# Optimization experiments

Hardware: AMD Instinct MI355X
Metric: run time of the kernel (lower is better)

## Reference

```python
import jax, jax.numpy as jnp
import numpy as np

B_SZ = 64            # oft_block_size
IN_F = 4096
OUT_F = 4096
R_IN = IN_F // B_SZ   # 64 blocks
R_OUT = OUT_F // B_SZ # 64 blocks
N_TRI = B_SZ * (B_SZ - 1) // 2  # 2016 packed strict-upper entries
NUM_NEUMANN = 5

_rows, _cols = np.triu_indices(B_SZ, k=1)
ROWS = jnp.asarray(_rows, dtype=jnp.int32)
COLS = jnp.asarray(_cols, dtype=jnp.int32)


def setup_inputs() -> dict:
    key = jax.random.key(0)
    k = jax.random.split(key, 5)
    x = jax.random.normal(k[0], (4, 2048, IN_F), dtype=jnp.float32)
    # small skew entries so the Neumann series approximates the Cayley transform
    Ro = jax.random.normal(k[1], (R_OUT, N_TRI), dtype=jnp.float32) * 0.01
    Ri = jax.random.normal(k[2], (R_IN, N_TRI), dtype=jnp.float32) * 0.01
    W = jax.random.normal(k[3], (OUT_F, IN_F), dtype=jnp.float32) * (1.0 / np.sqrt(IN_F))
    bias = jax.random.normal(k[4], (OUT_F,), dtype=jnp.float32) * 0.01
    rng = np.random.default_rng(0)
    perm_in = rng.permutation(IN_F)
    perm_in_inv = np.argsort(perm_in)
    perm_out = rng.permutation(OUT_F)
    return {
        "x": x, "Ro": Ro, "Ri": Ri, "W": W, "bias": bias,
        "perm_in_inv": jnp.asarray(perm_in_inv, dtype=jnp.int32),
        "perm_out": jnp.asarray(perm_out, dtype=jnp.int32),
    }


def _skew(vec):
    # vec: (r, n_tri) packed strict-upper entries -> (r, b, b) skew-symmetric
    r = vec.shape[0]
    M = jnp.zeros((r, B_SZ, B_SZ), dtype=vec.dtype).at[:, ROWS, COLS].set(vec)
    return M - jnp.swapaxes(M, -2, -1)


def _cayley_neumann(Q):
    # R = I + 2*(Q + Q^2 + Q^3 + Q^4)   (num_neumann_terms = 5)
    I = jnp.eye(B_SZ, dtype=Q.dtype)
    acc = Q
    Qp = Q
    for _ in range(3, NUM_NEUMANN):
        pass
    Q2 = jnp.matmul(Q, Q)
    acc = acc + Q2
    Qp = Q2
    for _ in range(3, NUM_NEUMANN):
        Qp = jnp.matmul(Qp, Q)
        acc = acc + Qp
    return I + 2.0 * acc


def reference(x, Ro, Ri, W, bias, perm_in_inv, perm_out):
    R_out = _cayley_neumann(_skew(Ro))   # (r_out, b, b)
    R_in = _cayley_neumann(_skew(Ri))    # (r_in, b, b)

    B, S, _ = x.shape
    xp = x[..., perm_in_inv]                               # input permutation
    xb = xp.reshape(B, S, R_IN, B_SZ)
    xR = jnp.einsum('bsrc,rcd->bsrd', xb, R_in)            # block-diag right rotate
    y = xR.reshape(B, S, IN_F) @ W.T + bias                # base linear
    yb = y.reshape(B, S, R_OUT, B_SZ)
    yR = jnp.einsum('bsrc,rcd->bsrd', yb, R_out)           # block-diag output rotate
    out = yR.reshape(B, S, OUT_F)[..., perm_out]           # output permutation
    return out
```

## Files before the change

kernel.cpp:

```cpp
#include <hip/hip_runtime.h>
#include <stdint.h>

#define IN_F 4096
#define OUT_F 4096
#define NTRI 2016

typedef unsigned short u16;
typedef __attribute__((ext_vector_type(8))) short short8;
typedef __attribute__((ext_vector_type(4))) float f32x4;
typedef __attribute__((ext_vector_type(4))) unsigned short u16x4;

__device__ __forceinline__ u16 f2bf(float f) {
    uint32_t u = __builtin_bit_cast(uint32_t, f);
    u = (u + 0x7FFFu + ((u >> 16) & 1u)) >> 16;
    return (u16)u;
}

__device__ __forceinline__ void gload16(const void* g, void* l) {
    __builtin_amdgcn_global_load_lds((__attribute__((address_space(1))) void*)g,
                                     (__attribute__((address_space(3))) void*)l,
                                     16, 0, 0);
}

#define FENCE() asm volatile("" ::: "memory")

__global__ void k_inv_perm(const int* __restrict__ perm_in_inv,
                           const int* __restrict__ perm_out,
                           int* __restrict__ pin, int* __restrict__ pinv_out) {
    int i = blockIdx.x * 256 + threadIdx.x;
    if (i < IN_F) {
        pin[perm_in_inv[i]] = i;
        pinv_out[perm_out[i]] = i;
    }
}

__global__ __launch_bounds__(256) void k_cayley(const float* __restrict__ Ro,
                                                const float* __restrict__ Ri,
                                                float* __restrict__ Rout,
                                                u16* __restrict__ QT16,
                                                u16* __restrict__ P16) {
    __shared__ __align__(16) float Qs[64 * 64];
    __shared__ __align__(16) float Ps[64 * 68];
    __shared__ __align__(16) float Ts[64 * 68];
    int b = blockIdx.x;
    const float* vec = (b < 64) ? (Ro + (size_t)b * NTRI) : (Ri + (size_t)(b - 64) * NTRI);
    int t = threadIdx.x;
    int tr = t >> 4, tc = t & 15;
#pragma unroll
    for (int e = 0; e < 16; ++e) {
        int el = e * 256 + t;
        int i = el >> 6, j = el & 63;
        float q = 0.f;
        if (i < j) q =  vec[i * 63 - (i * (i - 1)) / 2 + (j - i - 1)];
        if (i > j) q = -vec[j * 63 - (j * (j - 1)) / 2 + (i - j - 1)];
        Qs[el] = q;
    }
    __syncthreads();
    float a2[4][4], a3[4][4], a4[4][4];
#pragma unroll
    for (int i = 0; i < 4; ++i)
#pragma unroll
        for (int j = 0; j < 4; ++j) { a2[i][j] = 0.f; a3[i][j] = 0.f; a4[i][j] = 0.f; }
    for (int k = 0; k < 64; ++k) {
        f32x4 qa = *(const f32x4*)&Qs[k * 64 + tr * 4];
        f32x4 qb = *(const f32x4*)&Qs[k * 64 + tc * 4];
#pragma unroll
        for (int i = 0; i < 4; ++i)
#pragma unroll
            for (int j = 0; j < 4; ++j) a2[i][j] -= qa[i] * qb[j];
    }
#pragma unroll
    for (int i = 0; i < 4; ++i)
#pragma unroll
        for (int j = 0; j < 4; ++j) Ps[(tr * 4 + i) * 68 + tc * 4 + j] = a2[i][j];
    __syncthreads();
    for (int k = 0; k < 64; ++k) {
        f32x4 pa = *(const f32x4*)&Ps[k * 68 + tr * 4];
        f32x4 qb = *(const f32x4*)&Qs[k * 64 + tc * 4];
#pragma unroll
        for (int i = 0; i < 4; ++i)
#pragma unroll
            for (int j = 0; j < 4; ++j) a3[i][j] += pa[i] * qb[j];
    }
#pragma unroll
    for (int i = 0; i < 4; ++i)
#pragma unroll
        for (int j = 0; j < 4; ++j) Ts[(tc * 4 + j) * 68 + tr * 4 + i] = -a3[i][j];
    __syncthreads();
    for (int k = 0; k < 64; ++k) {
        f32x4 ta = *(const f32x4*)&Ts[k * 68 + tr * 4];
        f32x4 qb = *(const f32x4*)&Qs[k * 64 + tc * 4];
#pragma unroll
        for (int i = 0; i < 4; ++i)
#pragma unroll
            for (int j = 0; j < 4; ++j) a4[i][j] -= ta[i] * qb[j];
    }
    if (b < 64) {
        float* dst = Rout + (size_t)b * 4096;
        u16* qt = QT16 + (size_t)b * 4096;
#pragma unroll
        for (int i = 0; i < 4; ++i) {
            int gi = tr * 4 + i;
            f32x4 q4 = *(const f32x4*)&Qs[gi * 64 + tc * 4];
            f32x4 o;
#pragma unroll
            for (int j = 0; j < 4; ++j) {
                int gj = tc * 4 + j;
                o[j] = 2.f * (q4[j] + a2[i][j] + a3[i][j] + a4[i][j]) + ((gi == gj) ? 1.f : 0.f);
            }
            *(f32x4*)&dst[gi * 64 + tc * 4] = o;
#pragma unroll
            for (int j = 0; j < 4; ++j) qt[(tc * 4 + j) * 64 + gi] = f2bf(o[j]);
        }
    } else {
        u16* p = P16 + (size_t)(b - 64) * 4096;
#pragma unroll
        for (int i = 0; i < 4; ++i) {
            int gi = tr * 4 + i;
            f32x4 q4 = *(const f32x4*)&Qs[gi * 64 + tc * 4];
            u16x4 pk;
#pragma unroll
            for (int j = 0; j < 4; ++j) {
                int gj = tc * 4 + j;
                float v = 2.f * (q4[j] + a2[i][j] + a3[i][j] + a4[i][j]) + ((gi == gj) ? 1.f : 0.f);
                pk[j] = f2bf(v);
            }
            *(u16x4*)&p[gi * 64 + tc * 4] = pk;
        }
    }
}

__global__ void k_bias_rot(const float* __restrict__ bias, const float* __restrict__ Rout,
                           float* __restrict__ bias_prime) {
    int r = blockIdx.x;
    int d = threadIdx.x;
    const float* Rb = Rout + (size_t)r * 4096;
    float s = 0.f;
    for (int c = 0; c < 64; ++c) s += bias[r * 64 + c] * Rb[c * 64 + d];
    bias_prime[r * 64 + d] = s;
}

__global__ __launch_bounds__(256) void k_fold(const float* __restrict__ W,
                                              const u16* __restrict__ P16,
                                              const u16* __restrict__ QT16,
                                              const int* __restrict__ pinv_out,
                                              u16* __restrict__ Ctp) {
    __shared__ __align__(16) u16 Wst[128 * 64];
    __shared__ __align__(16) u16 Ut[64 * 128];
    const int s = blockIdx.x;
    const int br = blockIdx.y;
    const int t = threadIdx.x;
    const int lane = t & 63;
    const int w = t >> 6;
    const int fl = lane & 15;
    const int kg = lane >> 4;

    short8 bfP[4][2];
    const u16* Pbase = P16 + (size_t)s * 4096;
#pragma unroll
    for (int nf = 0; nf < 4; ++nf)
#pragma unroll
        for (int kk = 0; kk < 2; ++kk)
            bfP[nf][kk] = *(const short8*)(Pbase + (nf * 16 + fl) * 64 + kk * 32 + kg * 8);

#pragma unroll
    for (int q = 0; q < 4; ++q) {
        int ci = q * 256 + t;
        int row = ci >> 3, slot = ci & 7;
        const float* src = W + (size_t)(br * 128 + row) * IN_F + s * 64 + slot * 8;
        f32x4 v0 = *(const f32x4*)src;
        f32x4 v1 = *(const f32x4*)(src + 4);
        union { short8 v; u16 e[8]; } cv;
        cv.e[0] = f2bf(v0[0]); cv.e[1] = f2bf(v0[1]); cv.e[2] = f2bf(v0[2]); cv.e[3] = f2bf(v0[3]);
        cv.e[4] = f2bf(v1[0]); cv.e[5] = f2bf(v1[1]); cv.e[6] = f2bf(v1[2]); cv.e[7] = f2bf(v1[3]);
        *(short8*)&Wst[row * 64 + (slot ^ (row & 7)) * 8] = cv.v;
    }
    __syncthreads();

    f32x4 acc1[2][4];
#pragma unroll
    for (int mf = 0; mf < 2; ++mf)
#pragma unroll
        for (int nf = 0; nf < 4; ++nf) acc1[mf][nf] = f32x4{0.f, 0.f, 0.f, 0.f};
#pragma unroll
    for (int mf = 0; mf < 2; ++mf) {
        int row = w * 32 + mf * 16 + fl;
#pragma unroll
        for (int kk = 0; kk < 2; ++kk) {
            short8 a = *(const short8*)&Wst[row * 64 + ((kk * 4 + kg) ^ (row & 7)) * 8];
#pragma unroll
            for (int nf = 0; nf < 4; ++nf)
                acc1[mf][nf] = __builtin_amdgcn_mfma_f32_16x16x32_bf16(a, bfP[nf][kk], acc1[mf][nf], 0, 0, 0);
        }
    }
#pragma unroll
    for (int mf = 0; mf < 2; ++mf)
#pragma unroll
        for (int nf = 0; nf < 4; ++nf) {
            int i = nf * 16 + fl;
            int c = w * 32 + mf * 16 + kg * 4;
            u16x4 pk;
#pragma unroll
            for (int reg = 0; reg < 4; ++reg) pk[reg] = f2bf(acc1[mf][nf][reg]);
            int slot = c >> 3, half = (c >> 2) & 1;
            *(u16x4*)&Ut[i * 128 + ((slot ^ (i & 7)) << 3) + (half << 2)] = pk;
        }
    __syncthreads();

    const int rbl = w >> 1;
    const int r_g = br * 2 + rbl;
    short8 aQ[2][2];
#pragma unroll
    for (int mf2 = 0; mf2 < 2; ++mf2) {
        int d = (w & 1) * 32 + mf2 * 16 + fl;
#pragma unroll
        for (int kk = 0; kk < 2; ++kk)
            aQ[mf2][kk] = *(const short8*)(QT16 + (size_t)r_g * 4096 + d * 64 + kk * 32 + kg * 8);
    }
    f32x4 acc2[2][4];
#pragma unroll
    for (int mf2 = 0; mf2 < 2; ++mf2)
#pragma unroll
        for (int nf = 0; nf < 4; ++nf) acc2[mf2][nf] = f32x4{0.f, 0.f, 0.f, 0.f};
#pragma unroll
    for (int kk = 0; kk < 2; ++kk)
#pragma unroll
        for (int nf = 0; nf < 4; ++nf) {
            int i = nf * 16 + fl;
            int slot = rbl * 8 + kk * 4 + kg;
            short8 bu = *(const short8*)&Ut[i * 128 + ((slot ^ (i & 7)) << 3)];
#pragma unroll
            for (int mf2 = 0; mf2 < 2; ++mf2)
                acc2[mf2][nf] = __builtin_amdgcn_mfma_f32_16x16x32_bf16(aQ[mf2][kk], bu, acc2[mf2][nf], 0, 0, 0);
        }
#pragma unroll
    for (int mf2 = 0; mf2 < 2; ++mf2)
#pragma unroll
        for (int reg = 0; reg < 4; ++reg) {
            int o_g = br * 128 + w * 32 + mf2 * 16 + kg * 4 + reg;
            int j = pinv_out[o_g];
            u16* dst = Ctp + (size_t)j * IN_F + s * 64;
#pragma unroll
            for (int nf = 0; nf < 4; ++nf)
                dst[nf * 16 + fl] = f2bf(acc2[mf2][nf][reg]);
        }
}

__global__ __launch_bounds__(256) void k_permM(const u16* __restrict__ Ctp,
                                               const int* __restrict__ pin,
                                               u16* __restrict__ Mt) {
    __shared__ u16 row[4096];
    int j = blockIdx.x;
    int t = threadIdx.x;
    const u16* sr = Ctp + (size_t)j * IN_F;
#pragma unroll
    for (int e = 0; e < 16; ++e) row[e * 256 + t] = sr[e * 256 + t];
    __syncthreads();
    u16* dr = Mt + (size_t)j * IN_F;
#pragma unroll
    for (int e = 0; e < 16; ++e) {
        int k = e * 256 + t;
        dr[k] = row[pin[k]];
    }
}

__global__ void k_bias_perm(const float* __restrict__ bias_prime, const int* __restrict__ pout,
                            float* __restrict__ bias_final) {
    int j = blockIdx.x * 256 + threadIdx.x;
    if (j < OUT_F) bias_final[j] = bias_prime[pout[j]];
}

__global__ __launch_bounds__(256) void k_xcast(const float* __restrict__ x,
                                               u16* __restrict__ xb) {
    size_t idx = ((size_t)blockIdx.x * 256 + threadIdx.x) * 8;
    const f32x4* xp = (const f32x4*)(x + idx);
    f32x4 a = xp[0], b = xp[1];
    union { short8 v; u16 s[8]; } o;
    o.s[0] = f2bf(a[0]); o.s[1] = f2bf(a[1]); o.s[2] = f2bf(a[2]); o.s[3] = f2bf(a[3]);
    o.s[4] = f2bf(b[0]); o.s[5] = f2bf(b[1]); o.s[6] = f2bf(b[2]); o.s[7] = f2bf(b[3]);
    *(short8*)(xb + idx) = o.v;
}

__global__ __launch_bounds__(512, 2) void k_gemm(const u16* __restrict__ A,
                                                 const u16* __restrict__ Bt,
                                                 const float* __restrict__ bias,
                                                 float* __restrict__ out) {
    __shared__ __align__(16) u16 lds[65536];
    const int t = threadIdx.x;
    const int lane = t & 63;
    const int wid = t >> 6;
    const int wr = wid >> 2, wc = wid & 3;

    int flat = blockIdx.y * gridDim.x + blockIdx.x;
    int swz  = (flat & 7) * 64 + (flat >> 3);
    int bm = swz >> 4;
    int bn = swz & 15;

    const int srow = t >> 2;
    const int sks  = (t & 3) ^ ((t >> 3) & 3);
    const u16* sA0 = A  + (size_t)(bm * 256 + srow) * IN_F + sks * 8;
    const u16* sA1 = sA0 + (size_t)128 * IN_F;
    const u16* sB0 = Bt + (size_t)(bn * 256 + srow) * IN_F + sks * 8;
    const u16* sB1 = sB0 + (size_t)128 * IN_F;
    u16* dA = lds + t * 8;
    u16* dB = lds + 8192 + t * 8;

    const int frow = lane & 15;
    const int kg = lane >> 4;
    const int swzr = kg ^ ((frow >> 1) & 3);
    const int aoff = (wr * 128 + frow) * 32 + swzr * 8;
    const int boff = 8192 + (wc * 64 + frow) * 32 + swzr * 8;

    f32x4 acc[8][4];
#pragma unroll
    for (int m = 0; m < 8; ++m)
#pragma unroll
        for (int n = 0; n < 4; ++n) acc[m][n] = f32x4{0.f, 0.f, 0.f, 0.f};

#pragma unroll
    for (int p = 0; p < 3; ++p) {
        int off = p * 32;
        int bb = p * 16384;
        gload16(sA0 + off, dA + bb); gload16(sA1 + off, dA + bb + 4096);
        gload16(sB0 + off, dB + bb); gload16(sB1 + off, dB + bb + 4096);
    }
    asm volatile("s_waitcnt vmcnt(8)" ::: "memory");
    __builtin_amdgcn_s_barrier();
    FENCE();

    for (int t4 = 0; t4 < 128; t4 += 4) {
#pragma unroll
        for (int u = 0; u < 4; ++u) {
            const int kt = t4 + u;
            const u16* pa = lds + u * 16384 + aoff;
            const u16* pb = lds + u * 16384 + boff;
            int ts = kt + 3;
            int tsc = ts < 128 ? ts : 124;
            int off = tsc * 32;
            int bb = ((kt + 3) & 3) * 16384;
            short8 af0[4], bfr[4];
#pragma unroll
            for (int m = 0; m < 4; ++m) af0[m] = *(const short8*)(pa + m * 512);
#pragma unroll
            for (int n = 0; n < 4; ++n) bfr[n] = *(const short8*)(pb + n * 512);
            gload16(sA0 + off, dA + bb); gload16(sA1 + off, dA + bb + 4096);
            FENCE();
            __builtin_amdgcn_s_barrier();
            FENCE();
            __builtin_amdgcn_s_setprio(1);
#pragma unroll
            for (int m = 0; m < 4; ++m)
#pragma unroll
                for (int n = 0; n < 4; ++n)
                    acc[m][n] = __builtin_amdgcn_mfma_f32_16x16x32_bf16(af0[m], bfr[n], acc[m][n], 0, 0, 0);
            __builtin_amdgcn_s_setprio(0);
            FENCE();
            __builtin_amdgcn_s_barrier();
            FENCE();
            short8 af1[4];
#pragma unroll
            for (int m = 0; m < 4; ++m) af1[m] = *(const short8*)(pa + (m + 4) * 512);
            gload16(sB0 + off, dB + bb); gload16(sB1 + off, dB + bb + 4096);
            FENCE();
            __builtin_amdgcn_s_barrier();
            FENCE();
            __builtin_amdgcn_s_setprio(1);
#pragma unroll
            for (int m = 0; m < 4; ++m)
#pragma unroll
                for (int n = 0; n < 4; ++n)
                    acc[m + 4][n] = __builtin_amdgcn_mfma_f32_16x16x32_bf16(af1[m], bfr[n], acc[m + 4][n], 0, 0, 0);
            __builtin_amdgcn_s_setprio(0);
            asm volatile("s_waitcnt vmcnt(8)" ::: "memory");
            __builtin_amdgcn_s_barrier();
            FENCE();
        }
    }
    asm volatile("s_waitcnt vmcnt(0)" ::: "memory");

    const int col0 = bn * 256 + wc * 64 + frow;
    const int row0 = bm * 256 + wr * 128 + kg * 4;
    float bv[4];
#pragma unroll
    for (int n = 0; n < 4; ++n) bv[n] = bias[col0 + n * 16];
#pragma unroll
    for (int m = 0; m < 8; ++m)
#pragma unroll
        for (int n = 0; n < 4; ++n)
#pragma unroll
            for (int i = 0; i < 4; ++i)
                out[(size_t)(row0 + m * 16 + i) * OUT_F + col0 + n * 16] = acc[m][n][i] + bv[n];
}

extern "C" void kernel_launch(void* const* d_in, const int* in_sizes, int n_in,
                              void* d_out, int out_size, void* d_ws, size_t ws_size,
                              hipStream_t stream) {
    (void)in_sizes; (void)n_in; (void)out_size; (void)ws_size;
    const float* x    = (const float*)d_in[0];
    const float* Ro   = (const float*)d_in[1];
    const float* Ri   = (const float*)d_in[2];
    const float* W    = (const float*)d_in[3];
    const float* bias = (const float*)d_in[4];
    const int* perm_in_inv = (const int*)d_in[5];
    const int* perm_out    = (const int*)d_in[6];
    float* out = (float*)d_out;

    char* ws = (char*)d_ws;
    float* Rout   = (float*)(ws);
    u16*   P16    = (u16*)(ws + (1ull << 20));
    u16*   QT16   = (u16*)(ws + (1ull << 20) + (1 << 19));
    int*   pin    = (int*)(ws + (2ull << 20));
    int*   pinvo  = (int*)(ws + (2ull << 20) + (1 << 16));
    float* bprime = (float*)(ws + (2ull << 20) + (2 << 16));
    float* bfinal = (float*)(ws + (2ull << 20) + (3 << 16));
    u16*   Mt     = (u16*)(ws + (4ull << 20));
    u16*   xb     = (u16*)(ws + (36ull << 20));
    u16*   Ctp    = (u16*)(ws + (36ull << 20));

    k_inv_perm<<<16, 256, 0, stream>>>(perm_in_inv, perm_out, pin, pinvo);
    k_cayley<<<128, 256, 0, stream>>>(Ro, Ri, Rout, QT16, P16);
    k_bias_rot<<<64, 64, 0, stream>>>(bias, Rout, bprime);
    k_fold<<<dim3(64, 32), 256, 0, stream>>>(W, P16, QT16, pinvo, Ctp);
    k_permM<<<4096, 256, 0, stream>>>(Ctp, pin, Mt);
    k_bias_perm<<<16, 256, 0, stream>>>(bprime, perm_out, bfinal);
    k_xcast<<<16384, 256, 0, stream>>>(x, xb);
    k_gemm<<<dim3(16, 32), 512, 0, stream>>>(xb, Mt, bfinal, out);
}
```

Measured before the change: 333.9 us.

## Move input permutation into x cast, drop permM pass, rework GEMM pipeline

The input permutation now happens while x is cast to bf16, by gathering through LDS per row. This removes the separate pass that permuted the folded weight matrix (k_permM), and the bias rotation and permutation are merged into one kernel. The GEMM main loop moves from a 4-stage LDS ring with barriers inside each k-step to a 5-stage ring that processes two k-tiles per barrier with full 8x4 MFMA blocks. This cuts synchronisation per k-step at the cost of more LDS and larger register live ranges.

```diff
diff --git a/kernel.cpp b/kernel.cpp
--- a/kernel.cpp
+++ b/kernel.cpp
@@ -8,6 +8,7 @@
 typedef unsigned short u16;
 typedef __attribute__((ext_vector_type(8))) short short8;
 typedef __attribute__((ext_vector_type(4))) float f32x4;
+typedef __attribute__((ext_vector_type(4))) int i32x4;
 typedef __attribute__((ext_vector_type(4))) unsigned short u16x4;
 
 __device__ __forceinline__ u16 f2bf(float f) {
@@ -22,16 +23,9 @@
                                      16, 0, 0);
 }
 
-#define FENCE() asm volatile("" ::: "memory")
-
-__global__ void k_inv_perm(const int* __restrict__ perm_in_inv,
-                           const int* __restrict__ perm_out,
-                           int* __restrict__ pin, int* __restrict__ pinv_out) {
+__global__ void k_inv_perm(const int* __restrict__ perm_out, int* __restrict__ pinv_out) {
     int i = blockIdx.x * 256 + threadIdx.x;
-    if (i < IN_F) {
-        pin[perm_in_inv[i]] = i;
-        pinv_out[perm_out[i]] = i;
-    }
+    if (i < OUT_F) pinv_out[perm_out[i]] = i;
 }
 
 __global__ __launch_bounds__(256) void k_cayley(const float* __restrict__ Ro,
@@ -130,14 +124,17 @@
     }
 }
 
-__global__ void k_bias_rot(const float* __restrict__ bias, const float* __restrict__ Rout,
-                           float* __restrict__ bias_prime) {
-    int r = blockIdx.x;
-    int d = threadIdx.x;
+__global__ void k_bias(const float* __restrict__ bias, const float* __restrict__ Rout,
+                       const int* __restrict__ perm_out, float* __restrict__ bfinal) {
+    int j = blockIdx.x * 256 + threadIdx.x;
+    if (j >= OUT_F) return;
+    int o = perm_out[j];
+    int r = o >> 6, d = o & 63;
     const float* Rb = Rout + (size_t)r * 4096;
+    const float* bb = bias + r * 64;
     float s = 0.f;
-    for (int c = 0; c < 64; ++c) s += bias[r * 64 + c] * Rb[c * 64 + d];
-    bias_prime[r * 64 + d] = s;
+    for (int c = 0; c < 64; ++c) s += bb[c] * Rb[c * 64 + d];
+    bfinal[j] = s;
 }
 
 __global__ __launch_bounds__(256) void k_fold(const float* __restrict__ W,
@@ -246,46 +243,33 @@
         }
 }
 
-__global__ __launch_bounds__(256) void k_permM(const u16* __restrict__ Ctp,
-                                               const int* __restrict__ pin,
-                                               u16* __restrict__ Mt) {
-    __shared__ u16 row[4096];
-    int j = blockIdx.x;
-    int t = threadIdx.x;
-    const u16* sr = Ctp + (size_t)j * IN_F;
-#pragma unroll
-    for (int e = 0; e < 16; ++e) row[e * 256 + t] = sr[e * 256 + t];
-    __syncthreads();
-    u16* dr = Mt + (size_t)j * IN_F;
-#pragma unroll
-    for (int e = 0; e < 16; ++e) {
-        int k = e * 256 + t;
-        dr[k] = row[pin[k]];
-    }
-}
-
-__global__ void k_bias_perm(const float* __restrict__ bias_prime, const int* __restrict__ pout,
-                            float* __restrict__ bias_final) {
-    int j = blockIdx.x * 256 + threadIdx.x;
-    if (j < OUT_F) bias_final[j] = bias_prime[pout[j]];
-}
-
-__global__ __launch_bounds__(256) void k_xcast(const float* __restrict__ x,
-                                               u16* __restrict__ xb) {
-    size_t idx = ((size_t)blockIdx.x * 256 + threadIdx.x) * 8;
-    const f32x4* xp = (const f32x4*)(x + idx);
-    f32x4 a = xp[0], b = xp[1];
-    union { short8 v; u16 s[8]; } o;
-    o.s[0] = f2bf(a[0]); o.s[1] = f2bf(a[1]); o.s[2] = f2bf(a[2]); o.s[3] = f2bf(a[3]);
-    o.s[4] = f2bf(b[0]); o.s[5] = f2bf(b[1]); o.s[6] = f2bf(b[2]); o.s[7] = f2bf(b[3]);
-    *(short8*)(xb + idx) = o.v;
+__global__ __launch_bounds__(512) void k_xcast_perm(const float* __restrict__ x,
+                                                    const int* __restrict__ pii,
+                                                    u16* __restrict__ xb) {
+    __shared__ __align__(16) float xr[4096];
+    const int t = threadIdx.x;
+    int pv[8];
+    *(i32x4*)&pv[0] = *(const i32x4*)&pii[t * 8];
+    *(i32x4*)&pv[4] = *(const i32x4*)&pii[t * 8 + 4];
+    for (int r = 0; r < 8; ++r) {
+        size_t s = (size_t)blockIdx.x * 8 + r;
+        const float* src = x + s * 4096;
+        *(f32x4*)&xr[t * 4]        = *(const f32x4*)&src[t * 4];
+        *(f32x4*)&xr[2048 + t * 4] = *(const f32x4*)&src[2048 + t * 4];
+        __syncthreads();
+        union { short8 v; u16 e[8]; } o;
+#pragma unroll
+        for (int j = 0; j < 8; ++j) o.e[j] = f2bf(xr[pv[j]]);
+        *(short8*)&xb[s * 4096 + t * 8] = o.v;
+        __syncthreads();
+    }
 }
 
 __global__ __launch_bounds__(512, 2) void k_gemm(const u16* __restrict__ A,
                                                  const u16* __restrict__ Bt,
                                                  const float* __restrict__ bias,
                                                  float* __restrict__ out) {
-    __shared__ __align__(16) u16 lds[65536];
+    __shared__ __align__(16) u16 lds[81920];
     const int t = threadIdx.x;
     const int lane = t & 63;
     const int wid = t >> 6;
@@ -324,57 +308,60 @@
         gload16(sA0 + off, dA + bb); gload16(sA1 + off, dA + bb + 4096);
         gload16(sB0 + off, dB + bb); gload16(sB1 + off, dB + bb + 4096);
     }
-    asm volatile("s_waitcnt vmcnt(8)" ::: "memory");
+    asm volatile("s_waitcnt vmcnt(4)" ::: "memory");
     __builtin_amdgcn_s_barrier();
-    FENCE();
-
-    for (int t4 = 0; t4 < 128; t4 += 4) {
-#pragma unroll
-        for (int u = 0; u < 4; ++u) {
-            const int kt = t4 + u;
-            const u16* pa = lds + u * 16384 + aoff;
-            const u16* pb = lds + u * 16384 + boff;
+
+    int b0 = 0;
+    for (int p = 0; p < 64; ++p) {
+        const int kt = 2 * p;
+        int b1 = b0 + 1; if (b1 >= 5) b1 -= 5;
+        int s0 = b0 + 3; if (s0 >= 5) s0 -= 5;
+        int s1 = b0 + 4; if (s1 >= 5) s1 -= 5;
+        {
+            const u16* pa = lds + b0 * 16384 + aoff;
+            const u16* pb = lds + b0 * 16384 + boff;
+            short8 af[8], bf[4];
+#pragma unroll
+            for (int m = 0; m < 8; ++m) af[m] = *(const short8*)(pa + m * 512);
+#pragma unroll
+            for (int n = 0; n < 4; ++n) bf[n] = *(const short8*)(pb + n * 512);
             int ts = kt + 3;
-            int tsc = ts < 128 ? ts : 124;
-            int off = tsc * 32;
-            int bb = ((kt + 3) & 3) * 16384;
-            short8 af0[4], bfr[4];
-#pragma unroll
-            for (int m = 0; m < 4; ++m) af0[m] = *(const short8*)(pa + m * 512);
-#pragma unroll
-            for (int n = 0; n < 4; ++n) bfr[n] = *(const short8*)(pb + n * 512);
+            int off = (ts < 128 ? ts : 124) * 32;
+            int bb = s0 * 16384;
             gload16(sA0 + off, dA + bb); gload16(sA1 + off, dA + bb + 4096);
-            FENCE();
-            __builtin_amdgcn_s_barrier();
-            FENCE();
+            gload16(sB0 + off, dB + bb); gload16(sB1 + off, dB + bb + 4096);
             __builtin_amdgcn_s_setprio(1);
 #pragma unroll
-            for (int m = 0; m < 4; ++m)
+            for (int m = 0; m < 8; ++m)
 #pragma unroll
                 for (int n = 0; n < 4; ++n)
-                    acc[m][n] = __builtin_amdgcn_mfma_f32_16x16x32_bf16(af0[m], bfr[n], acc[m][n], 0, 0, 0);
+                    acc[m][n] = __builtin_amdgcn_mfma_f32_16x16x32_bf16(af[m], bf[n], acc[m][n], 0, 0, 0);
             __builtin_amdgcn_s_setprio(0);
-            FENCE();
-            __builtin_amdgcn_s_barrier();
-            FENCE();
-            short8 af1[4];
-#pragma unroll
-            for (int m = 0; m < 4; ++m) af1[m] = *(const short8*)(pa + (m + 4) * 512);
+        }
+        {
+            const u16* pa = lds + b1 * 16384 + aoff;
+            const u16* pb = lds + b1 * 16384 + boff;
+            short8 af[8], bf[4];
+#pragma unroll
+            for (int m = 0; m < 8; ++m) af[m] = *(const short8*)(pa + m * 512);
+#pragma unroll
+            for (int n = 0; n < 4; ++n) bf[n] = *(const short8*)(pb + n * 512);
+            int ts = kt + 4;
+            int off = (ts < 128 ? ts : 124) * 32;
+            int bb = s1 * 16384;
+            gload16(sA0 + off, dA + bb); gload16(sA1 + off, dA + bb + 4096);
             gload16(sB0 + off, dB + bb); gload16(sB1 + off, dB + bb + 4096);
-            FENCE();
-            __builtin_amdgcn_s_barrier();
-            FENCE();
             __builtin_amdgcn_s_setprio(1);
 #pragma unroll
-            for (int m = 0; m < 4; ++m)
+            for (int m = 0; m < 8; ++m)
 #pragma unroll
                 for (int n = 0; n < 4; ++n)
-                    acc[m + 4][n] = __builtin_amdgcn_mfma_f32_16x16x32_bf16(af1[m], bfr[n], acc[m + 4][n], 0, 0, 0);
+                    acc[m][n] = __builtin_amdgcn_mfma_f32_16x16x32_bf16(af[m], bf[n], acc[m][n], 0, 0, 0);
             __builtin_amdgcn_s_setprio(0);
-            asm volatile("s_waitcnt vmcnt(8)" ::: "memory");
-            __builtin_amdgcn_s_barrier();
-            FENCE();
-        }
+        }
+        asm volatile("s_waitcnt vmcnt(4)" ::: "memory");
+        __builtin_amdgcn_s_barrier();
+        b0 += 2; if (b0 >= 5) b0 -= 5;
     }
     asm volatile("s_waitcnt vmcnt(0)" ::: "memory");
 
@@ -409,20 +396,15 @@
     float* Rout   = (float*)(ws);
     u16*   P16    = (u16*)(ws + (1ull << 20));
     u16*   QT16   = (u16*)(ws + (1ull << 20) + (1 << 19));
-    int*   pin    = (int*)(ws + (2ull << 20));
-    int*   pinvo  = (int*)(ws + (2ull << 20) + (1 << 16));
-    float* bprime = (float*)(ws + (2ull << 20) + (2 << 16));
-    float* bfinal = (float*)(ws + (2ull << 20) + (3 << 16));
-    u16*   Mt     = (u16*)(ws + (4ull << 20));
+    int*   pinvo  = (int*)(ws + (2ull << 20));
+    float* bfinal = (float*)(ws + (2ull << 20) + (1 << 16));
+    u16*   Ctp    = (u16*)(ws + (4ull << 20));
     u16*   xb     = (u16*)(ws + (36ull << 20));
-    u16*   Ctp    = (u16*)(ws + (36ull << 20));
-
-    k_inv_perm<<<16, 256, 0, stream>>>(perm_in_inv, perm_out, pin, pinvo);
+
+    k_inv_perm<<<16, 256, 0, stream>>>(perm_out, pinvo);
     k_cayley<<<128, 256, 0, stream>>>(Ro, Ri, Rout, QT16, P16);
-    k_bias_rot<<<64, 64, 0, stream>>>(bias, Rout, bprime);
+    k_bias<<<16, 256, 0, stream>>>(bias, Rout, perm_out, bfinal);
     k_fold<<<dim3(64, 32), 256, 0, stream>>>(W, P16, QT16, pinvo, Ctp);
-    k_permM<<<4096, 256, 0, stream>>>(Ctp, pin, Mt);
-    k_bias_perm<<<16, 256, 0, stream>>>(bprime, perm_out, bfinal);
-    k_xcast<<<16384, 256, 0, stream>>>(x, xb);
-    k_gemm<<<dim3(16, 32), 512, 0, stream>>>(xb, Mt, bfinal, out);
-}
+    k_xcast_perm<<<1024, 512, 0, stream>>>(x, perm_in_inv, xb);
+    k_gemm<<<dim3(16, 32), 512, 0, stream>>>(xb, Ctp, bfinal, out);
+}
```

Result: no change. 335.2 us (+0.4%).
